# Kernel optimization log

Hardware: AMD Instinct MI355X
Metric: run time of the kernel (lower is better)

## Reference

```python
import jax, jax.numpy as jnp
import numpy as np

N_NODES = 50000
N_EDGES = 800000
N_GRAPHS = 64
IN_CH = 128
HID = 128
PROC_X = 128
Q_DIM = 768
PROC_Q = 128
OUT_CH = 32


def setup_inputs() -> dict:
    key = jax.random.key(0)
    ks = jax.random.split(key, 16)
    inp = {
        "x": jax.random.normal(ks[0], (N_NODES, IN_CH), dtype=jnp.float32),
        "edge_index": jax.random.randint(ks[1], (2, N_EDGES), 0, N_NODES, dtype=jnp.int64),
        "batch": jnp.sort(jax.random.randint(ks[2], (N_NODES,), 0, N_GRAPHS, dtype=jnp.int64)),
        "question_embedding": jax.random.normal(ks[3], (N_GRAPHS, Q_DIM), dtype=jnp.float32),
    }
    s = 1.0 / np.sqrt(HID)
    inp["W0"] = jax.random.uniform(ks[4], (IN_CH, HID), minval=-s, maxval=s)
    inp["b0"] = jnp.zeros((HID,), jnp.float32)
    inp["W1"] = jax.random.uniform(ks[5], (HID, HID), minval=-s, maxval=s)
    inp["b1"] = jnp.zeros((HID,), jnp.float32)
    inp["W2"] = jax.random.uniform(ks[6], (HID, PROC_X), minval=-s, maxval=s)
    inp["b2"] = jnp.zeros((PROC_X,), jnp.float32)
    inp["fc0_w"] = jax.random.uniform(ks[7], (Q_DIM, PROC_Q), minval=-s, maxval=s)
    inp["fc0_b"] = jnp.zeros((PROC_Q,), jnp.float32)
    inp["fc1_w"] = jax.random.uniform(ks[8], (PROC_X + PROC_Q, HID), minval=-s, maxval=s)
    inp["fc1_b"] = jnp.zeros((HID,), jnp.float32)
    inp["fc2_w"] = jax.random.uniform(ks[9], (HID, OUT_CH), minval=-s, maxval=s)
    inp["fc2_b"] = jnp.zeros((OUT_CH,), jnp.float32)
    return inp


def _gcn_norm(edge_index, n_nodes):
    """Add self-loops and compute symmetric GCN normalization per edge."""
    loop = jnp.arange(n_nodes, dtype=edge_index.dtype)
    src = jnp.concatenate([edge_index[0], loop])
    dst = jnp.concatenate([edge_index[1], loop])
    ones = jnp.ones_like(dst, dtype=jnp.float32)
    deg = jax.ops.segment_sum(ones, dst, num_segments=n_nodes)
    dinv = jnp.where(deg > 0, jax.lax.rsqrt(deg), 0.0)
    norm = dinv[src] * dinv[dst]  # [E+N]
    return src, dst, norm


def _gcn_conv(x, src, dst, norm, W, b):
    h = x @ W                                # [N, F_out]
    msg = h[src] * norm[:, None]             # gather + scale  [E+N, F_out]
    agg = jax.ops.segment_sum(msg, dst, num_segments=x.shape[0])
    return agg + b


def reference(x, edge_index, batch, question_embedding,
              W0, b0, W1, b1, W2, b2,
              fc0_w, fc0_b, fc1_w, fc1_b, fc2_w, fc2_b):
    n = x.shape[0]
    src, dst, norm = _gcn_norm(edge_index, n)
    h = jax.nn.relu(_gcn_conv(x, src, dst, norm, W0, b0))
    h = jax.nn.relu(_gcn_conv(h, src, dst, norm, W1, b1))
    h = jax.nn.relu(_gcn_conv(h, src, dst, norm, W2, b2))
    q = jax.nn.relu(question_embedding @ fc0_w + fc0_b)  # [G, PROC_Q]
    q_exp = q[batch]                                      # [N, PROC_Q]
    combined = jnp.concatenate([h, q_exp], axis=1)
    out = jax.nn.relu(combined @ fc1_w + fc1_b)
    out = out @ fc2_w + fc2_b
    return out
```

## Files before the change

### kernel.cpp

```cpp
#include <hip/hip_runtime.h>
#include <hip/hip_bf16.h>

#define N_NODES 50000
#define N_EDGES 800000
#define N_GRAPHS 64
#define LSTR 136

typedef __attribute__((ext_vector_type(4))) short s4v;
typedef __attribute__((ext_vector_type(8))) short s8v;
typedef __attribute__((ext_vector_type(16))) float f16v;

struct HL { short hi, lo; };

__device__ inline HL bsplit(float f) {
    HL r;
    unsigned u = __float_as_uint(f);
    unsigned rh = (u + 0x7FFFu + ((u >> 16) & 1u)) >> 16;
    r.hi = (short)rh;
    float fh = __uint_as_float(rh << 16);
    float fl = f - fh;
    unsigned u2 = __float_as_uint(fl);
    unsigned rl = (u2 + 0x7FFFu + ((u2 >> 16) & 1u)) >> 16;
    r.lo = (short)rl;
    return r;
}

__device__ inline unsigned short f2bf(float f) {
    unsigned u = __float_as_uint(f);
    return (unsigned short)((u + 0x7FFFu + ((u >> 16) & 1u)) >> 16);
}

__device__ inline float bflo(unsigned u) { return __uint_as_float(u << 16); }
__device__ inline float bfhi(unsigned u) { return __uint_as_float(u & 0xFFFF0000u); }

__device__ inline void gat8(const unsigned* __restrict__ Hs,
                            const unsigned short* __restrict__ colA,
                            int e, int l, float& a0, float& a1) {
    uint4 cw = *(const uint4*)(colA + e);
    unsigned u0 = Hs[(cw.x & 0xFFFFu) * 64u + l];
    unsigned u1 = Hs[(cw.x >> 16) * 64u + l];
    unsigned u2 = Hs[(cw.y & 0xFFFFu) * 64u + l];
    unsigned u3 = Hs[(cw.y >> 16) * 64u + l];
    unsigned u4 = Hs[(cw.z & 0xFFFFu) * 64u + l];
    unsigned u5 = Hs[(cw.z >> 16) * 64u + l];
    unsigned u6 = Hs[(cw.w & 0xFFFFu) * 64u + l];
    unsigned u7 = Hs[(cw.w >> 16) * 64u + l];
    a0 += ((bflo(u0) + bflo(u1)) + (bflo(u2) + bflo(u3)))
        + ((bflo(u4) + bflo(u5)) + (bflo(u6) + bflo(u7)));
    a1 += ((bfhi(u0) + bfhi(u1)) + (bfhi(u2) + bfhi(u3)))
        + ((bfhi(u4) + bfhi(u5)) + (bfhi(u6) + bfhi(u7)));
}


__global__ __launch_bounds__(512) void k_scan_a(const int* __restrict__ cnt,
                                                int* __restrict__ rowptr,
                                                int* __restrict__ bsum,
                                                float* __restrict__ dinv, int n) {
    __shared__ int s[512];
    int t = threadIdx.x;
    int i = blockIdx.x * 512 + t;
    int v = (i < n) ? cnt[i] : 0;
    if (i < n) dinv[i] = rsqrtf((float)(v + 1));
    int pv = (v + 7) & ~7;
    s[t] = pv;
    __syncthreads();
    for (int d = 1; d < 512; d <<= 1) {
        int x = (t >= d) ? s[t - d] : 0;
        __syncthreads();
        s[t] += x;
        __syncthreads();
    }
    if (i < n) rowptr[i] = s[t] - pv;
    if (t == 511) bsum[blockIdx.x] = s[511];
}

__global__ __launch_bounds__(512) void k_scan_c(int* __restrict__ rowptr,
                                                const int* __restrict__ bsum,
                                                int n, int nb) {
    __shared__ int sb[128];
    int t = threadIdx.x;
    if (t < 128) sb[t] = (t < nb) ? bsum[t] : 0;
    __syncthreads();
    for (int d = 1; d < 128; d <<= 1) {
        int x = 0;
        if (t < 128 && t >= d) x = sb[t - d];
        __syncthreads();
        if (t < 128) sb[t] += x;
        __syncthreads();
    }
    int add = (blockIdx.x > 0) ? sb[blockIdx.x - 1] : 0;
    int i = blockIdx.x * 512 + t;
    if (i < n) rowptr[i] += add;
    if (i == 0) rowptr[n] = sb[nb - 1];
}

__global__ __launch_bounds__(512) void k_prep(const float* __restrict__ qe,
                                              const float* __restrict__ fc0w,
                                              const float* __restrict__ fc0b,
                                              const float* __restrict__ fc1w,
                                              const float* __restrict__ fc1b,
                                              const float* __restrict__ W0,
                                              const float* __restrict__ W1,
                                              const float* __restrict__ W2,
                                              const float* __restrict__ fc2w,
                                              const int* __restrict__ ei,
                                              int* __restrict__ cnt,
                                              int* __restrict__ rank,
                                              short* __restrict__ WH,
                                              short* __restrict__ WL,
                                              unsigned* __restrict__ Hsd,
                                              unsigned short* __restrict__ colA,
                                              float* __restrict__ qq, int E) {
    int b = blockIdx.x, tid = threadIdx.x;
    if (b >= 482) {
        int e = (b - 482) * 512 + tid;
        if (e < E) rank[e] = atomicAdd(&cnt[ei[E + e]], 1);
        return;
    }
    if (b == 481) {
        if (tid < 64) Hsd[(unsigned)N_NODES * 64u + tid] = 0u;
        return;
    }
    if (b >= 200) {
        int idx = (b - 200) * 512 + tid;
        if (idx < 143752) {
            uint4 p;
            p.x = p.y = p.z = p.w = 0xC350C350u;
            ((uint4*)colA)[idx] = p;
        }
        return;
    }
    if (b >= 64) {
        int i = (b - 64) * 512 + tid;
        float val;
        int dst;
        if (i < 65536) {
            int mat = i >> 14, off = i & 16383;
            int k = off >> 7, n = off & 127;
            const float* src = (mat == 0) ? W0 : (mat == 1) ? W1 : (mat == 2) ? W2 : fc1w;
            val = src[k * 128 + n];
            dst = mat * 16384 + n * 128 + k;
        } else {
            int off = i - 65536;
            int k = off >> 5, n = off & 31;
            val = fc2w[k * 32 + n];
            dst = 65536 + n * 128 + k;
        }
        HL r = bsplit(val);
        WH[dst] = r.hi;
        WL[dst] = r.lo;
        return;
    }
    __shared__ float qs[768];
    __shared__ float red[512];
    __shared__ float ql[128];
    const float* fc1bot = fc1w + 128 * 128;
    int g = b;
    for (int i = tid; i < 768; i += 512) qs[i] = qe[g * 768 + i];
    __syncthreads();
    int j = tid & 127, sl = tid >> 7;
    int kb = sl * 192;
    float a0 = 0, a1 = 0, a2 = 0, a3 = 0;
    for (int k = 0; k < 192; k += 4) {
        a0 += qs[kb + k + 0] * fc0w[(kb + k + 0) * 128 + j];
        a1 += qs[kb + k + 1] * fc0w[(kb + k + 1) * 128 + j];
        a2 += qs[kb + k + 2] * fc0w[(kb + k + 2) * 128 + j];
        a3 += qs[kb + k + 3] * fc0w[(kb + k + 3) * 128 + j];
    }
    red[tid] = (a0 + a1) + (a2 + a3);
    __syncthreads();
    if (tid < 128)
        ql[tid] = fmaxf(((red[tid] + red[tid + 128]) + (red[tid + 256] + red[tid + 384]))
                        + fc0b[tid], 0.f);
    __syncthreads();
    kb = sl * 32;
    float b0 = 0, b1 = 0;
    for (int k = 0; k < 32; k += 2) {
        b0 += ql[kb + k + 0] * fc1bot[(kb + k + 0) * 128 + j];
        b1 += ql[kb + k + 1] * fc1bot[(kb + k + 1) * 128 + j];
    }
    red[tid] = b0 + b1;
    __syncthreads();
    if (tid < 128)
        qq[g * 128 + tid] = ((red[tid] + red[tid + 128]) + (red[tid + 256] + red[tid + 384]))
                            + fc1b[tid];
}

__global__ __launch_bounds__(128) void k_fg(const float* __restrict__ A32,
                                            const short* __restrict__ WTh,
                                            const short* __restrict__ WTl,
                                            const float* __restrict__ dinv,
                                            unsigned short* __restrict__ oHs,
                                            const int* __restrict__ ei,
                                            const int* __restrict__ rowptr,
                                            const int* __restrict__ rank,
                                            unsigned short* __restrict__ colA,
                                            int nrows, int E, int GG) {
    const int tid = threadIdx.x;
    if (blockIdx.x >= GG) {
        int e = (blockIdx.x - GG) * 128 + tid;
        if (e < E) colA[rowptr[ei[E + e]] + rank[e]] = (unsigned short)ei[e];
        return;
    }
    __shared__ short Ah[32 * LSTR];
    const int row0 = blockIdx.x * 32;

    #pragma unroll
    for (int i = 0; i < 8; ++i) {
        int u = i * 128 + tid;
        int r = u >> 5, c4 = u & 31;
        int gr = row0 + r;
        float4 v = make_float4(0.f, 0.f, 0.f, 0.f);
        if (gr < nrows) v = ((const float4*)A32)[(size_t)gr * 32 + c4];
        s4v h4 = {(short)f2bf(v.x), (short)f2bf(v.y), (short)f2bf(v.z), (short)f2bf(v.w)};
        *(s4v*)&Ah[r * LSTR + c4 * 4] = h4;
    }
    __syncthreads();

    const int wv = tid >> 6, lane = tid & 63;
    const int m = lane & 31, half = lane >> 5;
    const int c0 = wv * 64 + m;
    f16v acc0 = {0.f}, acc1 = {0.f};
    #pragma unroll
    for (int ks = 0; ks < 8; ++ks) {
        int ko = ks * 16 + half * 8;
        s8v ah  = *(const s8v*)&Ah[m * LSTR + ko];
        s8v bh0 = *(const s8v*)&WTh[(size_t)c0 * 128 + ko];
        s8v bl0 = *(const s8v*)&WTl[(size_t)c0 * 128 + ko];
        s8v bh1 = *(const s8v*)&WTh[(size_t)(c0 + 32) * 128 + ko];
        s8v bl1 = *(const s8v*)&WTl[(size_t)(c0 + 32) * 128 + ko];
        acc0 = __builtin_amdgcn_mfma_f32_32x32x16_bf16(ah, bh0, acc0, 0, 0, 0);
        acc0 = __builtin_amdgcn_mfma_f32_32x32x16_bf16(ah, bl0, acc0, 0, 0, 0);
        acc1 = __builtin_amdgcn_mfma_f32_32x32x16_bf16(ah, bh1, acc1, 0, 0, 0);
        acc1 = __builtin_amdgcn_mfma_f32_32x32x16_bf16(ah, bl1, acc1, 0, 0, 0);
    }

    #pragma unroll
    for (int reg = 0; reg < 16; ++reg) {
        int rl = (reg & 3) + 8 * (reg >> 2) + 4 * half;
        int gr = row0 + rl;
        if (gr >= nrows) continue;
        float sc = dinv[gr];
        oHs[(size_t)gr * 128 + c0]      = f2bf(acc0[reg] * sc);
        oHs[(size_t)gr * 128 + c0 + 32] = f2bf(acc1[reg] * sc);
    }
}

template <int FC>
__global__ __launch_bounds__(512) void k_gg(const unsigned* __restrict__ Hs,
                                            const int* __restrict__ rowptr,
                                            const unsigned short* __restrict__ colA,
                                            const float* __restrict__ dinv,
                                            const float* __restrict__ bias,
                                            const short* __restrict__ WTh,
                                            const short* __restrict__ WTl,
                                            const short* __restrict__ W2h,
                                            const short* __restrict__ W2l,
                                            const float* __restrict__ qq,
                                            const int* __restrict__ batch,
                                            const float* __restrict__ fc2b,
                                            unsigned short* __restrict__ oHs,
                                            float* __restrict__ out,
                                            int n) {
    __shared__ short Ah[32 * LSTR];
    __shared__ short Pl[FC ? 32 * LSTR : 1];
    __shared__ float red[FC ? 3 * 32 * 33 : 1];
    const int tid = threadIdx.x;
    const int row0 = blockIdx.x * 32;
    const int wv = tid >> 6, l = tid & 63;
    const int m = l & 31, half = l >> 5;

    const float2 bb = ((const float2*)bias)[l];
    for (int i = 0; i < 4; ++i) {
        int r = wv * 4 + i;
        int node = row0 + r;
        unsigned pack = 0;
        if (node < n) {
            int e0 = __builtin_amdgcn_readfirstlane(rowptr[node]);
            int e1 = __builtin_amdgcn_readfirstlane(rowptr[node + 1]);
            float a0 = 0.f, a1 = 0.f, c0v = 0.f, c1v = 0.f;
            int e = e0;
            for (; e + 16 <= e1; e += 16) {
                gat8(Hs, colA, e, l, a0, a1);
                gat8(Hs, colA, e + 8, l, c0v, c1v);
            }
            for (; e < e1; e += 8)
                gat8(Hs, colA, e, l, a0, a1);
            a0 += c0v;
            a1 += c1v;
            float di = dinv[node];
            unsigned uh = Hs[(unsigned)node * 64u + l];
            float o0 = fmaxf((a0 + bflo(uh)) * di + bb.x, 0.f);
            float o1 = fmaxf((a1 + bfhi(uh)) * di + bb.y, 0.f);
            pack = (unsigned)f2bf(o0) | ((unsigned)f2bf(o1) << 16);
        }
        ((unsigned*)Ah)[r * 68 + l] = pack;
    }
    __syncthreads();

    const int c0 = wv * 32 + m;
    f16v acc = {0.f};
    if (wv < 4) {
        #pragma unroll
        for (int ks = 0; ks < 8; ++ks) {
            int ko = ks * 16 + half * 8;
            s8v ah = *(const s8v*)&Ah[m * LSTR + ko];
            s8v bh = *(const s8v*)&WTh[(size_t)c0 * 128 + ko];
            s8v bl = *(const s8v*)&WTl[(size_t)c0 * 128 + ko];
            acc = __builtin_amdgcn_mfma_f32_32x32x16_bf16(ah, bh, acc, 0, 0, 0);
            acc = __builtin_amdgcn_mfma_f32_32x32x16_bf16(ah, bl, acc, 0, 0, 0);
        }
    }

    if (FC == 0) {
        if (wv < 4) {
            #pragma unroll
            for (int reg = 0; reg < 16; ++reg) {
                int rl = (reg & 3) + 8 * (reg >> 2) + 4 * half;
                int gr = row0 + rl;
                if (gr >= n) continue;
                oHs[(size_t)gr * 128 + c0] = f2bf(acc[reg] * dinv[gr]);
            }
        }
    } else {
        __syncthreads();
        if (wv < 4) {
            #pragma unroll
            for (int reg = 0; reg < 16; ++reg) {
                int rl = (reg & 3) + 8 * (reg >> 2) + 4 * half;
                int gr = row0 + rl;
                int g = (gr < n) ? batch[gr] : 0;
                float v = fmaxf(acc[reg] + qq[(size_t)g * 128 + c0], 0.f);
                HL p = bsplit(v);
                Ah[rl * LSTR + c0] = p.hi;
                Pl[rl * LSTR + c0] = p.lo;
            }
        }
        __syncthreads();
        f16v acc2 = {0.f};
        if (wv < 4) {
            #pragma unroll
            for (int ks = 0; ks < 2; ++ks) {
                int ko = wv * 32 + ks * 16 + half * 8;
                s8v ah = *(const s8v*)&Ah[m * LSTR + ko];
                s8v al = *(const s8v*)&Pl[m * LSTR + ko];
                s8v bh = *(const s8v*)&W2h[(size_t)m * 128 + ko];
                s8v bl = *(const s8v*)&W2l[(size_t)m * 128 + ko];
                acc2 = __builtin_amdgcn_mfma_f32_32x32x16_bf16(ah, bh, acc2, 0, 0, 0);
                acc2 = __builtin_amdgcn_mfma_f32_32x32x16_bf16(ah, bl, acc2, 0, 0, 0);
                acc2 = __builtin_amdgcn_mfma_f32_32x32x16_bf16(al, bh, acc2, 0, 0, 0);
            }
            if (wv > 0) {
                #pragma unroll
                for (int reg = 0; reg < 16; ++reg) {
                    int rl = (reg & 3) + 8 * (reg >> 2) + 4 * half;
                    red[(wv - 1) * 1056 + rl * 33 + m] = acc2[reg];
                }
            }
        }
        __syncthreads();
        if (wv == 0) {
            #pragma unroll
            for (int reg = 0; reg < 16; ++reg) {
                int rl = (reg & 3) + 8 * (reg >> 2) + 4 * half;
                int gr = row0 + rl;
                if (gr < n)
                    out[(size_t)gr * 32 + m] = acc2[reg]
                        + (red[rl * 33 + m] + red[1056 + rl * 33 + m])
                        + red[2112 + rl * 33 + m] + fc2b[m];
            }
        }
    }
}


extern "C" void kernel_launch(void* const* d_in, const int* in_sizes, int n_in,
                              void* d_out, int out_size, void* d_ws, size_t ws_size,
                              hipStream_t stream) {
    const float* x    = (const float*)d_in[0];
    const int*   ei   = (const int*)d_in[1];
    const int*   batch= (const int*)d_in[2];
    const float* qe   = (const float*)d_in[3];
    const float* W0   = (const float*)d_in[4];
    const float* b0   = (const float*)d_in[5];
    const float* W1   = (const float*)d_in[6];
    const float* b1   = (const float*)d_in[7];
    const float* W2   = (const float*)d_in[8];
    const float* b2   = (const float*)d_in[9];
    const float* fc0w = (const float*)d_in[10];
    const float* fc0b = (const float*)d_in[11];
    const float* fc1w = (const float*)d_in[12];
    const float* fc1b = (const float*)d_in[13];
    const float* fc2w = (const float*)d_in[14];
    const float* fc2b = (const float*)d_in[15];
    float* out = (float*)d_out;

    float* WS = (float*)d_ws;
    unsigned short* HS  = (unsigned short*)WS;
    unsigned short* HS2 = (unsigned short*)(WS + 3200064);
    float* DINV = WS + 6400128;
    float* QQ   = WS + 6450144;
    int*   CNT  = (int*)(WS + 6458336);
    int*   ROWPTR = (int*)(WS + 6508352);
    int*   RANK = (int*)(WS + 6558368);
    unsigned short* COL = (unsigned short*)(WS + 7358368);
    int*   BSUM = (int*)(WS + 7933376);
    short* WTH  = (short*)(WS + 7933504);
    short* WTL  = WTH + 69632;

    const int N = N_NODES, E = N_EDGES;
    const int sb = (N + 511) / 512;
    const int gg = (N + 31) / 32;
    const int histb = (E + 511) / 512;
    const int fillb = (E + 127) / 128;

    (void)hipMemsetAsync(CNT, 0, N * sizeof(int), stream);
    k_prep<<<482 + histb, 512, 0, stream>>>(qe, fc0w, fc0b, fc1w, fc1b,
                                            W0, W1, W2, fc2w, ei, CNT, RANK,
                                            WTH, WTL, (unsigned*)HS, COL, QQ, E);
    k_scan_a<<<sb, 512, 0, stream>>>(CNT, ROWPTR, BSUM, DINV, N);
    k_scan_c<<<sb, 512, 0, stream>>>(ROWPTR, BSUM, N, sb);
    k_fg<<<gg + fillb, 128, 0, stream>>>(x, WTH, WTL, DINV, HS,
                                         ei, ROWPTR, RANK, COL, N, E, gg);
    k_gg<0><<<gg, 512, 0, stream>>>((const unsigned*)HS, ROWPTR, COL, DINV, b0,
                                    WTH + 16384, WTL + 16384, nullptr, nullptr,
                                    nullptr, nullptr, nullptr, HS2, nullptr, N);
    k_gg<0><<<gg, 512, 0, stream>>>((const unsigned*)HS2, ROWPTR, COL, DINV, b1,
                                    WTH + 32768, WTL + 32768, nullptr, nullptr,
                                    nullptr, nullptr, nullptr, HS, nullptr, N);
    k_gg<1><<<gg, 512, 0, stream>>>((const unsigned*)HS, ROWPTR, COL, DINV, b2,
                                    WTH + 49152, WTL + 49152, WTH + 65536, WTL + 65536,
                                    QQ, batch, fc2b, nullptr, out, N);
}
```

Measured before the change: 310.0 us.

## Restructure GCN gather to vectorized 16B-per-lane loads with prefetch and 256-thread blocks

Rewrites the sparse aggregation in the fused GCN layer kernel. Each lane now loads 16 bytes (8 bf16 features), so one wave covers four neighbor rows per pass, and partial sums are combined with cross-lane shuffles. The next neighbor-index word and the next node's self feature are prefetched to hide latency. Row pointers and dinv are loaded once per wave and broadcast with readlane. Blocks shrink from 512 to 256 threads with an occupancy hint, and all four waves now do MFMA work instead of half idling. The extra shuffle reductions and the zeroing of an additional padding row in the setup kernel are the added cost.

```diff
diff --git a/kernel.cpp b/kernel.cpp
--- a/kernel.cpp
+++ b/kernel.cpp
@@ -32,24 +32,6 @@
 
 __device__ inline float bflo(unsigned u) { return __uint_as_float(u << 16); }
 __device__ inline float bfhi(unsigned u) { return __uint_as_float(u & 0xFFFF0000u); }
-
-__device__ inline void gat8(const unsigned* __restrict__ Hs,
-                            const unsigned short* __restrict__ colA,
-                            int e, int l, float& a0, float& a1) {
-    uint4 cw = *(const uint4*)(colA + e);
-    unsigned u0 = Hs[(cw.x & 0xFFFFu) * 64u + l];
-    unsigned u1 = Hs[(cw.x >> 16) * 64u + l];
-    unsigned u2 = Hs[(cw.y & 0xFFFFu) * 64u + l];
-    unsigned u3 = Hs[(cw.y >> 16) * 64u + l];
-    unsigned u4 = Hs[(cw.z & 0xFFFFu) * 64u + l];
-    unsigned u5 = Hs[(cw.z >> 16) * 64u + l];
-    unsigned u6 = Hs[(cw.w & 0xFFFFu) * 64u + l];
-    unsigned u7 = Hs[(cw.w >> 16) * 64u + l];
-    a0 += ((bflo(u0) + bflo(u1)) + (bflo(u2) + bflo(u3)))
-        + ((bflo(u4) + bflo(u5)) + (bflo(u6) + bflo(u7)));
-    a1 += ((bfhi(u0) + bfhi(u1)) + (bfhi(u2) + bfhi(u3)))
-        + ((bfhi(u4) + bfhi(u5)) + (bfhi(u6) + bfhi(u7)));
-}
 
 
 __global__ __launch_bounds__(512) void k_scan_a(const int* __restrict__ cnt,
@@ -119,6 +101,7 @@
     }
     if (b == 481) {
         if (tid < 64) Hsd[(unsigned)N_NODES * 64u + tid] = 0u;
+        if (tid >= 64 && tid < 128) Hsd[100001u * 64u + (unsigned)(tid - 64)] = 0u;
         return;
     }
     if (b >= 200) {
@@ -247,115 +230,179 @@
 }
 
 template <int FC>
-__global__ __launch_bounds__(512) void k_gg(const unsigned* __restrict__ Hs,
-                                            const int* __restrict__ rowptr,
-                                            const unsigned short* __restrict__ colA,
-                                            const float* __restrict__ dinv,
-                                            const float* __restrict__ bias,
-                                            const short* __restrict__ WTh,
-                                            const short* __restrict__ WTl,
-                                            const short* __restrict__ W2h,
-                                            const short* __restrict__ W2l,
-                                            const float* __restrict__ qq,
-                                            const int* __restrict__ batch,
-                                            const float* __restrict__ fc2b,
-                                            unsigned short* __restrict__ oHs,
-                                            float* __restrict__ out,
-                                            int n) {
-    __shared__ short Ah[32 * LSTR];
-    __shared__ short Pl[FC ? 32 * LSTR : 1];
-    __shared__ float red[FC ? 3 * 32 * 33 : 1];
+__global__ __launch_bounds__(256, 7) void k_gg(const unsigned* __restrict__ Hs,
+                                               const int* __restrict__ rowptr,
+                                               const unsigned short* __restrict__ colA,
+                                               const float* __restrict__ dinv,
+                                               const float* __restrict__ bias,
+                                               const short* __restrict__ WTh,
+                                               const short* __restrict__ WTl,
+                                               const short* __restrict__ W2h,
+                                               const short* __restrict__ W2l,
+                                               const float* __restrict__ qq,
+                                               const int* __restrict__ batch,
+                                               const float* __restrict__ fc2b,
+                                               unsigned short* __restrict__ oHs,
+                                               float* __restrict__ out,
+                                               int n) {
+    __shared__ short SM[(FC ? 64 : 32) * LSTR];
+    short* Ah = SM;
     const int tid = threadIdx.x;
     const int row0 = blockIdx.x * 32;
     const int wv = tid >> 6, l = tid & 63;
     const int m = l & 31, half = l >> 5;
-
-    const float2 bb = ((const float2*)bias)[l];
-    for (int i = 0; i < 4; ++i) {
-        int r = wv * 4 + i;
-        int node = row0 + r;
-        unsigned pack = 0;
-        if (node < n) {
-            int e0 = __builtin_amdgcn_readfirstlane(rowptr[node]);
-            int e1 = __builtin_amdgcn_readfirstlane(rowptr[node + 1]);
-            float a0 = 0.f, a1 = 0.f, c0v = 0.f, c1v = 0.f;
-            int e = e0;
-            for (; e + 16 <= e1; e += 16) {
-                gat8(Hs, colA, e, l, a0, a1);
-                gat8(Hs, colA, e + 8, l, c0v, c1v);
+    const int il = l & 15;
+    const unsigned ilo = (unsigned)(il * 4);
+    const unsigned shq = (l & 16) ? 16u : 0u;
+    const bool qhi = (l & 32) != 0;
+    const bool q0 = (l < 16);
+
+    int pidx = row0 + wv * 8 + l;
+    if (pidx > N_NODES) pidx = N_NODES;
+    const int rp = rowptr[pidx];
+    const int dvu = (int)__float_as_uint(dinv[pidx < N_NODES ? pidx : N_NODES - 1]);
+
+    const float4 bA = ((const float4*)bias)[il * 2];
+    const float4 bB = ((const float4*)bias)[il * 2 + 1];
+
+    int node = row0 + wv * 8;
+    int e0 = __builtin_amdgcn_readlane(rp, 0);
+    int e1 = __builtin_amdgcn_readlane(rp, 1);
+    bool alive = node < n;
+    bool act = alive && (e0 < e1);
+    uint4 cw = {0, 0, 0, 0}, sf = {0, 0, 0, 0};
+    if (alive) sf = *(const uint4*)(Hs + (unsigned)node * 64u + ilo);
+    if (act)   cw = *(const uint4*)(colA + e0);
+
+    for (int i = 0; i < 8; ++i) {
+        float a0 = 0, a1 = 0, a2 = 0, a3 = 0, a4 = 0, a5 = 0, a6 = 0, a7 = 0;
+        float c0f = 0, c1f = 0, c2f = 0, c3f = 0, c4f = 0, c5f = 0, c6f = 0, c7f = 0;
+        if (act) {
+            int e = e0 + 8;
+            uint4 cur = cw;
+            while (true) {
+                const bool more = e < e1;
+                uint4 nx = {0, 0, 0, 0};
+                if (more) nx = *(const uint4*)(colA + e);
+                unsigned wA = qhi ? cur.y : cur.x;
+                unsigned wB = qhi ? cur.w : cur.z;
+                unsigned ca = (wA >> shq) & 0xFFFFu;
+                unsigned cb = (wB >> shq) & 0xFFFFu;
+                uint4 va = *(const uint4*)(Hs + ca * 64u + ilo);
+                uint4 vb = *(const uint4*)(Hs + cb * 64u + ilo);
+                a0 += bflo(va.x); a1 += bfhi(va.x);
+                a2 += bflo(va.y); a3 += bfhi(va.y);
+                a4 += bflo(va.z); a5 += bfhi(va.z);
+                a6 += bflo(va.w); a7 += bfhi(va.w);
+                c0f += bflo(vb.x); c1f += bfhi(vb.x);
+                c2f += bflo(vb.y); c3f += bfhi(vb.y);
+                c4f += bflo(vb.z); c5f += bfhi(vb.z);
+                c6f += bflo(vb.w); c7f += bfhi(vb.w);
+                if (!more) break;
+                cur = nx; e += 8;
             }
-            for (; e < e1; e += 8)
-                gat8(Hs, colA, e, l, a0, a1);
-            a0 += c0v;
-            a1 += c1v;
-            float di = dinv[node];
-            unsigned uh = Hs[(unsigned)node * 64u + l];
-            float o0 = fmaxf((a0 + bflo(uh)) * di + bb.x, 0.f);
-            float o1 = fmaxf((a1 + bfhi(uh)) * di + bb.y, 0.f);
-            pack = (unsigned)f2bf(o0) | ((unsigned)f2bf(o1) << 16);
-        }
-        ((unsigned*)Ah)[r * 68 + l] = pack;
+        }
+        float s0 = a0 + c0f, s1 = a1 + c1f, s2 = a2 + c2f, s3 = a3 + c3f;
+        float s4 = a4 + c4f, s5 = a5 + c5f, s6 = a6 + c6f, s7 = a7 + c7f;
+
+        int e0n = e1;
+        int e1n = (i < 7) ? __builtin_amdgcn_readlane(rp, i + 2) : 0;
+        int noden = node + 1;
+        bool aliven = (i < 7) && (noden < n);
+        bool actn = aliven && (e0n < e1n);
+        uint4 cwn = {0, 0, 0, 0}, sfn = {0, 0, 0, 0};
+        if (aliven) sfn = *(const uint4*)(Hs + (unsigned)noden * 64u + ilo);
+        if (actn)   cwn = *(const uint4*)(colA + e0n);
+
+        const int r = wv * 8 + i;
+        if (alive) {
+            s0 += __shfl_xor(s0, 16); s1 += __shfl_xor(s1, 16);
+            s2 += __shfl_xor(s2, 16); s3 += __shfl_xor(s3, 16);
+            s4 += __shfl_xor(s4, 16); s5 += __shfl_xor(s5, 16);
+            s6 += __shfl_xor(s6, 16); s7 += __shfl_xor(s7, 16);
+            s0 += __shfl_xor(s0, 32); s1 += __shfl_xor(s1, 32);
+            s2 += __shfl_xor(s2, 32); s3 += __shfl_xor(s3, 32);
+            s4 += __shfl_xor(s4, 32); s5 += __shfl_xor(s5, 32);
+            s6 += __shfl_xor(s6, 32); s7 += __shfl_xor(s7, 32);
+            float di = __uint_as_float((unsigned)__builtin_amdgcn_readlane(dvu, i));
+            float o0 = fmaxf((s0 + bflo(sf.x)) * di + bA.x, 0.f);
+            float o1 = fmaxf((s1 + bfhi(sf.x)) * di + bA.y, 0.f);
+            float o2 = fmaxf((s2 + bflo(sf.y)) * di + bA.z, 0.f);
+            float o3 = fmaxf((s3 + bfhi(sf.y)) * di + bA.w, 0.f);
+            float o4 = fmaxf((s4 + bflo(sf.z)) * di + bB.x, 0.f);
+            float o5 = fmaxf((s5 + bfhi(sf.z)) * di + bB.y, 0.f);
+            float o6 = fmaxf((s6 + bflo(sf.w)) * di + bB.z, 0.f);
+            float o7 = fmaxf((s7 + bfhi(sf.w)) * di + bB.w, 0.f);
+            if (q0) {
+                uint4 pk;
+                pk.x = (unsigned)f2bf(o0) | ((unsigned)f2bf(o1) << 16);
+                pk.y = (unsigned)f2bf(o2) | ((unsigned)f2bf(o3) << 16);
+                pk.z = (unsigned)f2bf(o4) | ((unsigned)f2bf(o5) << 16);
+                pk.w = (unsigned)f2bf(o6) | ((unsigned)f2bf(o7) << 16);
+                *(uint4*)&Ah[r * LSTR + il * 8] = pk;
+            }
+        } else if (q0) {
+            uint4 z = {0, 0, 0, 0};
+            *(uint4*)&Ah[r * LSTR + il * 8] = z;
+        }
+        e0 = e0n; e1 = e1n; cw = cwn; sf = sfn;
+        act = actn; alive = aliven; node = noden;
     }
     __syncthreads();
 
     const int c0 = wv * 32 + m;
     f16v acc = {0.f};
-    if (wv < 4) {
+    #pragma unroll
+    for (int ks = 0; ks < 8; ++ks) {
+        int ko = ks * 16 + half * 8;
+        s8v ah = *(const s8v*)&Ah[m * LSTR + ko];
+        s8v bh = *(const s8v*)&WTh[(size_t)c0 * 128 + ko];
+        s8v bl = *(const s8v*)&WTl[(size_t)c0 * 128 + ko];
+        acc = __builtin_amdgcn_mfma_f32_32x32x16_bf16(ah, bh, acc, 0, 0, 0);
+        acc = __builtin_amdgcn_mfma_f32_32x32x16_bf16(ah, bl, acc, 0, 0, 0);
+    }
+
+    if (FC == 0) {
         #pragma unroll
-        for (int ks = 0; ks < 8; ++ks) {
-            int ko = ks * 16 + half * 8;
+        for (int reg = 0; reg < 16; ++reg) {
+            int rl = (reg & 3) + 8 * (reg >> 2) + 4 * half;
+            int gr = row0 + rl;
+            if (gr >= n) continue;
+            oHs[(size_t)gr * 128 + c0] = f2bf(acc[reg] * dinv[gr]);
+        }
+    } else {
+        short* Pl = SM + 32 * LSTR;
+        __syncthreads();
+        #pragma unroll
+        for (int reg = 0; reg < 16; ++reg) {
+            int rl = (reg & 3) + 8 * (reg >> 2) + 4 * half;
+            int gr = row0 + rl;
+            int g = (gr < n) ? batch[gr] : 0;
+            float v = fmaxf(acc[reg] + qq[(size_t)g * 128 + c0], 0.f);
+            HL p = bsplit(v);
+            Ah[rl * LSTR + c0] = p.hi;
+            Pl[rl * LSTR + c0] = p.lo;
+        }
+        __syncthreads();
+        f16v acc2 = {0.f};
+        #pragma unroll
+        for (int ks = 0; ks < 2; ++ks) {
+            int ko = wv * 32 + ks * 16 + half * 8;
             s8v ah = *(const s8v*)&Ah[m * LSTR + ko];
-            s8v bh = *(const s8v*)&WTh[(size_t)c0 * 128 + ko];
-            s8v bl = *(const s8v*)&WTl[(size_t)c0 * 128 + ko];
-            acc = __builtin_amdgcn_mfma_f32_32x32x16_bf16(ah, bh, acc, 0, 0, 0);
-            acc = __builtin_amdgcn_mfma_f32_32x32x16_bf16(ah, bl, acc, 0, 0, 0);
-        }
-    }
-
-    if (FC == 0) {
-        if (wv < 4) {
+            s8v al = *(const s8v*)&Pl[m * LSTR + ko];
+            s8v bh = *(const s8v*)&W2h[(size_t)m * 128 + ko];
+            s8v bl = *(const s8v*)&W2l[(size_t)m * 128 + ko];
+            acc2 = __builtin_amdgcn_mfma_f32_32x32x16_bf16(ah, bh, acc2, 0, 0, 0);
+            acc2 = __builtin_amdgcn_mfma_f32_32x32x16_bf16(ah, bl, acc2, 0, 0, 0);
+            acc2 = __builtin_amdgcn_mfma_f32_32x32x16_bf16(al, bh, acc2, 0, 0, 0);
+        }
+        __syncthreads();
+        float* red = (float*)SM;
+        if (wv > 0) {
             #pragma unroll
             for (int reg = 0; reg < 16; ++reg) {
                 int rl = (reg & 3) + 8 * (reg >> 2) + 4 * half;
-                int gr = row0 + rl;
-                if (gr >= n) continue;
-                oHs[(size_t)gr * 128 + c0] = f2bf(acc[reg] * dinv[gr]);
-            }
-        }
-    } else {
-        __syncthreads();
-        if (wv < 4) {
-            #pragma unroll
-            for (int reg = 0; reg < 16; ++reg) {
-                int rl = (reg & 3) + 8 * (reg >> 2) + 4 * half;
-                int gr = row0 + rl;
-                int g = (gr < n) ? batch[gr] : 0;
-                float v = fmaxf(acc[reg] + qq[(size_t)g * 128 + c0], 0.f);
-                HL p = bsplit(v);
-                Ah[rl * LSTR + c0] = p.hi;
-                Pl[rl * LSTR + c0] = p.lo;
-            }
-        }
-        __syncthreads();
-        f16v acc2 = {0.f};
-        if (wv < 4) {
-            #pragma unroll
-            for (int ks = 0; ks < 2; ++ks) {
-                int ko = wv * 32 + ks * 16 + half * 8;
-                s8v ah = *(const s8v*)&Ah[m * LSTR + ko];
-                s8v al = *(const s8v*)&Pl[m * LSTR + ko];
-                s8v bh = *(const s8v*)&W2h[(size_t)m * 128 + ko];
-                s8v bl = *(const s8v*)&W2l[(size_t)m * 128 + ko];
-                acc2 = __builtin_amdgcn_mfma_f32_32x32x16_bf16(ah, bh, acc2, 0, 0, 0);
-                acc2 = __builtin_amdgcn_mfma_f32_32x32x16_bf16(ah, bl, acc2, 0, 0, 0);
-                acc2 = __builtin_amdgcn_mfma_f32_32x32x16_bf16(al, bh, acc2, 0, 0, 0);
-            }
-            if (wv > 0) {
-                #pragma unroll
-                for (int reg = 0; reg < 16; ++reg) {
-                    int rl = (reg & 3) + 8 * (reg >> 2) + 4 * half;
-                    red[(wv - 1) * 1056 + rl * 33 + m] = acc2[reg];
-                }
+                red[(wv - 1) * 1056 + rl * 33 + m] = acc2[reg];
             }
         }
         __syncthreads();
@@ -422,13 +469,13 @@
     k_scan_c<<<sb, 512, 0, stream>>>(ROWPTR, BSUM, N, sb);
     k_fg<<<gg + fillb, 128, 0, stream>>>(x, WTH, WTL, DINV, HS,
                                          ei, ROWPTR, RANK, COL, N, E, gg);
-    k_gg<0><<<gg, 512, 0, stream>>>((const unsigned*)HS, ROWPTR, COL, DINV, b0,
+    k_gg<0><<<gg, 256, 0, stream>>>((const unsigned*)HS, ROWPTR, COL, DINV, b0,
                                     WTH + 16384, WTL + 16384, nullptr, nullptr,
                                     nullptr, nullptr, nullptr, HS2, nullptr, N);
-    k_gg<0><<<gg, 512, 0, stream>>>((const unsigned*)HS2, ROWPTR, COL, DINV, b1,
+    k_gg<0><<<gg, 256, 0, stream>>>((const unsigned*)HS2, ROWPTR, COL, DINV, b1,
                                     WTH + 32768, WTL + 32768, nullptr, nullptr,
                                     nullptr, nullptr, nullptr, HS, nullptr, N);
-    k_gg<1><<<gg, 512, 0, stream>>>((const unsigned*)HS, ROWPTR, COL, DINV, b2,
+    k_gg<1><<<gg, 256, 0, stream>>>((const unsigned*)HS, ROWPTR, COL, DINV, b2,
                                     WTH + 49152, WTL + 49152, WTH + 65536, WTL + 65536,
                                     QQ, batch, fc2b, nullptr, out, N);
 }
```

Measured after the change: 307.6 us. Within noise of the previous version (-0.8%).

## Gather four nodes per wave with 16-byte loads and shrink k_gg blocks to 256

Applied to the files above, without the earlier changes.

Restructures the SpMM gather so each wave handles four nodes at once: 16 lanes per node, each loading a uint4 (8 bf16 features) per neighbor, instead of one node per wave with 4-byte loads per lane. Neighbor index groups are prefetched one step ahead, and inactive lanes are redirected to a zeroed padding row so the wave loop stays uniform. Blocks shrink from 512 to 256 threads, and the idle waves that sat out the MFMA stage are removed. The LDS buffers are merged into one shared array and the reduction buffer reuses it. The aim is more memory-level parallelism and wider transactions in the bandwidth-bound gather, at the cost of more divergence when degrees within a wave differ.

```diff
diff --git a/kernel.cpp b/kernel.cpp
--- a/kernel.cpp
+++ b/kernel.cpp
@@ -32,24 +32,6 @@
 
 __device__ inline float bflo(unsigned u) { return __uint_as_float(u << 16); }
 __device__ inline float bfhi(unsigned u) { return __uint_as_float(u & 0xFFFF0000u); }
-
-__device__ inline void gat8(const unsigned* __restrict__ Hs,
-                            const unsigned short* __restrict__ colA,
-                            int e, int l, float& a0, float& a1) {
-    uint4 cw = *(const uint4*)(colA + e);
-    unsigned u0 = Hs[(cw.x & 0xFFFFu) * 64u + l];
-    unsigned u1 = Hs[(cw.x >> 16) * 64u + l];
-    unsigned u2 = Hs[(cw.y & 0xFFFFu) * 64u + l];
-    unsigned u3 = Hs[(cw.y >> 16) * 64u + l];
-    unsigned u4 = Hs[(cw.z & 0xFFFFu) * 64u + l];
-    unsigned u5 = Hs[(cw.z >> 16) * 64u + l];
-    unsigned u6 = Hs[(cw.w & 0xFFFFu) * 64u + l];
-    unsigned u7 = Hs[(cw.w >> 16) * 64u + l];
-    a0 += ((bflo(u0) + bflo(u1)) + (bflo(u2) + bflo(u3)))
-        + ((bflo(u4) + bflo(u5)) + (bflo(u6) + bflo(u7)));
-    a1 += ((bfhi(u0) + bfhi(u1)) + (bfhi(u2) + bfhi(u3)))
-        + ((bfhi(u4) + bfhi(u5)) + (bfhi(u6) + bfhi(u7)));
-}
 
 
 __global__ __launch_bounds__(512) void k_scan_a(const int* __restrict__ cnt,
@@ -119,6 +101,7 @@
     }
     if (b == 481) {
         if (tid < 64) Hsd[(unsigned)N_NODES * 64u + tid] = 0u;
+        if (tid >= 64 && tid < 128) Hsd[100001u * 64u + (unsigned)(tid - 64)] = 0u;
         return;
     }
     if (b >= 200) {
@@ -247,115 +230,164 @@
 }
 
 template <int FC>
-__global__ __launch_bounds__(512) void k_gg(const unsigned* __restrict__ Hs,
-                                            const int* __restrict__ rowptr,
-                                            const unsigned short* __restrict__ colA,
-                                            const float* __restrict__ dinv,
-                                            const float* __restrict__ bias,
-                                            const short* __restrict__ WTh,
-                                            const short* __restrict__ WTl,
-                                            const short* __restrict__ W2h,
-                                            const short* __restrict__ W2l,
-                                            const float* __restrict__ qq,
-                                            const int* __restrict__ batch,
-                                            const float* __restrict__ fc2b,
-                                            unsigned short* __restrict__ oHs,
-                                            float* __restrict__ out,
-                                            int n) {
-    __shared__ short Ah[32 * LSTR];
-    __shared__ short Pl[FC ? 32 * LSTR : 1];
-    __shared__ float red[FC ? 3 * 32 * 33 : 1];
+__global__ __launch_bounds__(256, 7) void k_gg(const unsigned* __restrict__ Hs,
+                                               const int* __restrict__ rowptr,
+                                               const unsigned short* __restrict__ colA,
+                                               const float* __restrict__ dinv,
+                                               const float* __restrict__ bias,
+                                               const short* __restrict__ WTh,
+                                               const short* __restrict__ WTl,
+                                               const short* __restrict__ W2h,
+                                               const short* __restrict__ W2l,
+                                               const float* __restrict__ qq,
+                                               const int* __restrict__ batch,
+                                               const float* __restrict__ fc2b,
+                                               unsigned short* __restrict__ oHs,
+                                               float* __restrict__ out,
+                                               int n) {
+    __shared__ short SM[(FC ? 64 : 32) * LSTR];
+    short* Ah = SM;
     const int tid = threadIdx.x;
     const int row0 = blockIdx.x * 32;
     const int wv = tid >> 6, l = tid & 63;
     const int m = l & 31, half = l >> 5;
-
-    const float2 bb = ((const float2*)bias)[l];
-    for (int i = 0; i < 4; ++i) {
-        int r = wv * 4 + i;
-        int node = row0 + r;
-        unsigned pack = 0;
-        if (node < n) {
-            int e0 = __builtin_amdgcn_readfirstlane(rowptr[node]);
-            int e1 = __builtin_amdgcn_readfirstlane(rowptr[node + 1]);
-            float a0 = 0.f, a1 = 0.f, c0v = 0.f, c1v = 0.f;
-            int e = e0;
-            for (; e + 16 <= e1; e += 16) {
-                gat8(Hs, colA, e, l, a0, a1);
-                gat8(Hs, colA, e + 8, l, c0v, c1v);
-            }
-            for (; e < e1; e += 8)
-                gat8(Hs, colA, e, l, a0, a1);
-            a0 += c0v;
-            a1 += c1v;
-            float di = dinv[node];
-            unsigned uh = Hs[(unsigned)node * 64u + l];
-            float o0 = fmaxf((a0 + bflo(uh)) * di + bb.x, 0.f);
-            float o1 = fmaxf((a1 + bfhi(uh)) * di + bb.y, 0.f);
-            pack = (unsigned)f2bf(o0) | ((unsigned)f2bf(o1) << 16);
-        }
-        ((unsigned*)Ah)[r * 68 + l] = pack;
+    const int il = l & 15;
+    const int q = l >> 4;
+    const unsigned ilo = (unsigned)(il * 4);
+
+    const int nodeA = row0 + wv * 8 + q;
+    const int nodeB = nodeA + 4;
+    const int eA0 = rowptr[min(nodeA, n)];
+    const int eA1 = rowptr[min(nodeA + 1, n)];
+    const int eB0 = rowptr[min(nodeB, n)];
+    const int eB1 = rowptr[min(nodeB + 1, n)];
+
+    #pragma unroll
+    for (int r = 0; r < 2; ++r) {
+        const int node = r ? nodeB : nodeA;
+        const int e0 = r ? eB0 : eA0;
+        const int e1 = r ? eB1 : eA1;
+        const bool alive = node < n;
+        const int rl = wv * 8 + r * 4 + q;
+
+        uint4 sf = *(const uint4*)(Hs + (unsigned)min(node, n) * 64u + ilo);
+        uint4 cw = *(const uint4*)(colA + e0);
+
+        float ac0 = 0, ac1 = 0, ac2 = 0, ac3 = 0;
+        float ac4 = 0, ac5 = 0, ac6 = 0, ac7 = 0;
+        const int ng = (e1 - e0) >> 3;
+        int g = 0;
+        while (__any(g < ng)) {
+            const bool act = g < ng;
+            const uint4 cur = cw;
+            if (g + 1 < ng) cw = *(const uint4*)(colA + e0 + (g + 1) * 8);
+            unsigned i0 = act ? (cur.x & 0xFFFFu) : 50000u;
+            unsigned i1 = act ? (cur.x >> 16)     : 50000u;
+            unsigned i2 = act ? (cur.y & 0xFFFFu) : 50000u;
+            unsigned i3 = act ? (cur.y >> 16)     : 50000u;
+            unsigned i4 = act ? (cur.z & 0xFFFFu) : 50000u;
+            unsigned i5 = act ? (cur.z >> 16)     : 50000u;
+            unsigned i6 = act ? (cur.w & 0xFFFFu) : 50000u;
+            unsigned i7 = act ? (cur.w >> 16)     : 50000u;
+            uint4 v0 = *(const uint4*)(Hs + i0 * 64u + ilo);
+            uint4 v1 = *(const uint4*)(Hs + i1 * 64u + ilo);
+            uint4 v2 = *(const uint4*)(Hs + i2 * 64u + ilo);
+            uint4 v3 = *(const uint4*)(Hs + i3 * 64u + ilo);
+            uint4 v4 = *(const uint4*)(Hs + i4 * 64u + ilo);
+            uint4 v5 = *(const uint4*)(Hs + i5 * 64u + ilo);
+            uint4 v6 = *(const uint4*)(Hs + i6 * 64u + ilo);
+            uint4 v7 = *(const uint4*)(Hs + i7 * 64u + ilo);
+            ac0 += ((bflo(v0.x) + bflo(v1.x)) + (bflo(v2.x) + bflo(v3.x)))
+                 + ((bflo(v4.x) + bflo(v5.x)) + (bflo(v6.x) + bflo(v7.x)));
+            ac1 += ((bfhi(v0.x) + bfhi(v1.x)) + (bfhi(v2.x) + bfhi(v3.x)))
+                 + ((bfhi(v4.x) + bfhi(v5.x)) + (bfhi(v6.x) + bfhi(v7.x)));
+            ac2 += ((bflo(v0.y) + bflo(v1.y)) + (bflo(v2.y) + bflo(v3.y)))
+                 + ((bflo(v4.y) + bflo(v5.y)) + (bflo(v6.y) + bflo(v7.y)));
+            ac3 += ((bfhi(v0.y) + bfhi(v1.y)) + (bfhi(v2.y) + bfhi(v3.y)))
+                 + ((bfhi(v4.y) + bfhi(v5.y)) + (bfhi(v6.y) + bfhi(v7.y)));
+            ac4 += ((bflo(v0.z) + bflo(v1.z)) + (bflo(v2.z) + bflo(v3.z)))
+                 + ((bflo(v4.z) + bflo(v5.z)) + (bflo(v6.z) + bflo(v7.z)));
+            ac5 += ((bfhi(v0.z) + bfhi(v1.z)) + (bfhi(v2.z) + bfhi(v3.z)))
+                 + ((bfhi(v4.z) + bfhi(v5.z)) + (bfhi(v6.z) + bfhi(v7.z)));
+            ac6 += ((bflo(v0.w) + bflo(v1.w)) + (bflo(v2.w) + bflo(v3.w)))
+                 + ((bflo(v4.w) + bflo(v5.w)) + (bflo(v6.w) + bflo(v7.w)));
+            ac7 += ((bfhi(v0.w) + bfhi(v1.w)) + (bfhi(v2.w) + bfhi(v3.w)))
+                 + ((bfhi(v4.w) + bfhi(v5.w)) + (bfhi(v6.w) + bfhi(v7.w)));
+            ++g;
+        }
+        const float4 bA = ((const float4*)bias)[il * 2];
+        const float4 bB = ((const float4*)bias)[il * 2 + 1];
+        const float di = dinv[min(node, n - 1)];
+        float o0 = fmaxf((ac0 + bflo(sf.x)) * di + bA.x, 0.f);
+        float o1 = fmaxf((ac1 + bfhi(sf.x)) * di + bA.y, 0.f);
+        float o2 = fmaxf((ac2 + bflo(sf.y)) * di + bA.z, 0.f);
+        float o3 = fmaxf((ac3 + bfhi(sf.y)) * di + bA.w, 0.f);
+        float o4 = fmaxf((ac4 + bflo(sf.z)) * di + bB.x, 0.f);
+        float o5 = fmaxf((ac5 + bfhi(sf.z)) * di + bB.y, 0.f);
+        float o6 = fmaxf((ac6 + bflo(sf.w)) * di + bB.z, 0.f);
+        float o7 = fmaxf((ac7 + bfhi(sf.w)) * di + bB.w, 0.f);
+        uint4 pk;
+        pk.x = alive ? ((unsigned)f2bf(o0) | ((unsigned)f2bf(o1) << 16)) : 0u;
+        pk.y = alive ? ((unsigned)f2bf(o2) | ((unsigned)f2bf(o3) << 16)) : 0u;
+        pk.z = alive ? ((unsigned)f2bf(o4) | ((unsigned)f2bf(o5) << 16)) : 0u;
+        pk.w = alive ? ((unsigned)f2bf(o6) | ((unsigned)f2bf(o7) << 16)) : 0u;
+        *(uint4*)&Ah[rl * LSTR + il * 8] = pk;
     }
     __syncthreads();
 
     const int c0 = wv * 32 + m;
     f16v acc = {0.f};
-    if (wv < 4) {
+    #pragma unroll
+    for (int ks = 0; ks < 8; ++ks) {
+        int ko = ks * 16 + half * 8;
+        s8v ah = *(const s8v*)&Ah[m * LSTR + ko];
+        s8v bh = *(const s8v*)&WTh[(size_t)c0 * 128 + ko];
+        s8v bl = *(const s8v*)&WTl[(size_t)c0 * 128 + ko];
+        acc = __builtin_amdgcn_mfma_f32_32x32x16_bf16(ah, bh, acc, 0, 0, 0);
+        acc = __builtin_amdgcn_mfma_f32_32x32x16_bf16(ah, bl, acc, 0, 0, 0);
+    }
+
+    if (FC == 0) {
         #pragma unroll
-        for (int ks = 0; ks < 8; ++ks) {
-            int ko = ks * 16 + half * 8;
+        for (int reg = 0; reg < 16; ++reg) {
+            int rl = (reg & 3) + 8 * (reg >> 2) + 4 * half;
+            int gr = row0 + rl;
+            if (gr >= n) continue;
+            oHs[(size_t)gr * 128 + c0] = f2bf(acc[reg] * dinv[gr]);
+        }
+    } else {
+        short* Pl = SM + 32 * LSTR;
+        __syncthreads();
+        #pragma unroll
+        for (int reg = 0; reg < 16; ++reg) {
+            int rl = (reg & 3) + 8 * (reg >> 2) + 4 * half;
+            int gr = row0 + rl;
+            int g = (gr < n) ? batch[gr] : 0;
+            float v = fmaxf(acc[reg] + qq[(size_t)g * 128 + c0], 0.f);
+            HL p = bsplit(v);
+            Ah[rl * LSTR + c0] = p.hi;
+            Pl[rl * LSTR + c0] = p.lo;
+        }
+        __syncthreads();
+        f16v acc2 = {0.f};
+        #pragma unroll
+        for (int ks = 0; ks < 2; ++ks) {
+            int ko = wv * 32 + ks * 16 + half * 8;
             s8v ah = *(const s8v*)&Ah[m * LSTR + ko];
-            s8v bh = *(const s8v*)&WTh[(size_t)c0 * 128 + ko];
-            s8v bl = *(const s8v*)&WTl[(size_t)c0 * 128 + ko];
-            acc = __builtin_amdgcn_mfma_f32_32x32x16_bf16(ah, bh, acc, 0, 0, 0);
-            acc = __builtin_amdgcn_mfma_f32_32x32x16_bf16(ah, bl, acc, 0, 0, 0);
-        }
-    }
-
-    if (FC == 0) {
-        if (wv < 4) {
+            s8v al = *(const s8v*)&Pl[m * LSTR + ko];
+            s8v bh = *(const s8v*)&W2h[(size_t)m * 128 + ko];
+            s8v bl = *(const s8v*)&W2l[(size_t)m * 128 + ko];
+            acc2 = __builtin_amdgcn_mfma_f32_32x32x16_bf16(ah, bh, acc2, 0, 0, 0);
+            acc2 = __builtin_amdgcn_mfma_f32_32x32x16_bf16(ah, bl, acc2, 0, 0, 0);
+            acc2 = __builtin_amdgcn_mfma_f32_32x32x16_bf16(al, bh, acc2, 0, 0, 0);
+        }
+        __syncthreads();
+        float* red = (float*)SM;
+        if (wv > 0) {
             #pragma unroll
             for (int reg = 0; reg < 16; ++reg) {
                 int rl = (reg & 3) + 8 * (reg >> 2) + 4 * half;
-                int gr = row0 + rl;
-                if (gr >= n) continue;
-                oHs[(size_t)gr * 128 + c0] = f2bf(acc[reg] * dinv[gr]);
-            }
-        }
-    } else {
-        __syncthreads();
-        if (wv < 4) {
-            #pragma unroll
-            for (int reg = 0; reg < 16; ++reg) {
-                int rl = (reg & 3) + 8 * (reg >> 2) + 4 * half;
-                int gr = row0 + rl;
-                int g = (gr < n) ? batch[gr] : 0;
-                float v = fmaxf(acc[reg] + qq[(size_t)g * 128 + c0], 0.f);
-                HL p = bsplit(v);
-                Ah[rl * LSTR + c0] = p.hi;
-                Pl[rl * LSTR + c0] = p.lo;
-            }
-        }
-        __syncthreads();
-        f16v acc2 = {0.f};
-        if (wv < 4) {
-            #pragma unroll
-            for (int ks = 0; ks < 2; ++ks) {
-                int ko = wv * 32 + ks * 16 + half * 8;
-                s8v ah = *(const s8v*)&Ah[m * LSTR + ko];
-                s8v al = *(const s8v*)&Pl[m * LSTR + ko];
-                s8v bh = *(const s8v*)&W2h[(size_t)m * 128 + ko];
-                s8v bl = *(const s8v*)&W2l[(size_t)m * 128 + ko];
-                acc2 = __builtin_amdgcn_mfma_f32_32x32x16_bf16(ah, bh, acc2, 0, 0, 0);
-                acc2 = __builtin_amdgcn_mfma_f32_32x32x16_bf16(ah, bl, acc2, 0, 0, 0);
-                acc2 = __builtin_amdgcn_mfma_f32_32x32x16_bf16(al, bh, acc2, 0, 0, 0);
-            }
-            if (wv > 0) {
-                #pragma unroll
-                for (int reg = 0; reg < 16; ++reg) {
-                    int rl = (reg & 3) + 8 * (reg >> 2) + 4 * half;
-                    red[(wv - 1) * 1056 + rl * 33 + m] = acc2[reg];
-                }
+                red[(wv - 1) * 1056 + rl * 33 + m] = acc2[reg];
             }
         }
         __syncthreads();
@@ -422,13 +454,13 @@
     k_scan_c<<<sb, 512, 0, stream>>>(ROWPTR, BSUM, N, sb);
     k_fg<<<gg + fillb, 128, 0, stream>>>(x, WTH, WTL, DINV, HS,
                                          ei, ROWPTR, RANK, COL, N, E, gg);
-    k_gg<0><<<gg, 512, 0, stream>>>((const unsigned*)HS, ROWPTR, COL, DINV, b0,
+    k_gg<0><<<gg, 256, 0, stream>>>((const unsigned*)HS, ROWPTR, COL, DINV, b0,
                                     WTH + 16384, WTL + 16384, nullptr, nullptr,
                                     nullptr, nullptr, nullptr, HS2, nullptr, N);
-    k_gg<0><<<gg, 512, 0, stream>>>((const unsigned*)HS2, ROWPTR, COL, DINV, b1,
+    k_gg<0><<<gg, 256, 0, stream>>>((const unsigned*)HS2, ROWPTR, COL, DINV, b1,
                                     WTH + 32768, WTL + 32768, nullptr, nullptr,
                                     nullptr, nullptr, nullptr, HS, nullptr, N);
-    k_gg<1><<<gg, 512, 0, stream>>>((const unsigned*)HS, ROWPTR, COL, DINV, b2,
+    k_gg<1><<<gg, 256, 0, stream>>>((const unsigned*)HS, ROWPTR, COL, DINV, b2,
                                     WTH + 49152, WTL + 49152, WTH + 65536, WTL + 65536,
                                     QQ, batch, fc2b, nullptr, out, N);
 }
```

Result: slower. 332.1 us (+7.1%).
